# Optimization experiments

Hardware: AMD Instinct MI355X
Metric: run time of the kernel (lower is better)

Reference implementation:

```python
import jax, jax.numpy as jnp
import numpy as np

B, L, K = 256, 128, 6
FA, FB, D = 39, 10, 128
R, T = 3, 2
NEG = -9e8


def _gru(x, h, wih, whh, bih, bhh):
    # torch.nn.GRUCell semantics
    gi = x @ wih.T + bih
    gh = h @ whh.T + bhh
    ir, iz, inn = jnp.split(gi, 3, axis=-1)
    hr, hz, hn = jnp.split(gh, 3, axis=-1)
    r = jax.nn.sigmoid(ir + hr)
    z = jax.nn.sigmoid(iz + hz)
    n = jnp.tanh(inn + r * hn)
    return (1.0 - z) * n + z * h


def _forward(atom_list, bond_list, atom_mask, atom_fc_w, atom_fc_b, nbr_fc_w, nbr_fc_b,
             align_w, align_b, attend_w, attend_b, gru_wih, gru_whh, gru_bih, gru_bhh,
             mol_align_w, mol_align_b, mol_attend_w, mol_attend_b,
             mol_gru_wih, mol_gru_whh, mol_gru_bih, mol_gru_bhh, out_w, out_b,
             atom_degree_list, bond_degree_list):
    lrelu = jax.nn.leaky_relu  # slope 0.01, matches torch default
    bidx = jnp.arange(atom_list.shape[0])[:, None, None]
    gather = lambda f, idx: f[bidx, idx]  # [B,L,F] gathered by [B,L,K] -> [B,L,K,F]

    atom_feature = lrelu(atom_list @ atom_fc_w + atom_fc_b)  # [B,L,D]
    nbr = jnp.concatenate([gather(atom_list, atom_degree_list),
                           gather(bond_list, bond_degree_list)], axis=-1)
    nbr = lrelu(nbr @ nbr_fc_w + nbr_fc_b)  # [B,L,K,D]

    pad = atom_list.shape[1] - 1  # mol_length-1 is padding sentinel
    attend_mask = (atom_degree_list != pad).astype(atom_feature.dtype)[..., None]
    softmax_mask = jnp.where(atom_degree_list == pad, NEG, 0.0).astype(atom_feature.dtype)[..., None]

    def attn(cur, nbr_feat, aw, ab, tw, tb):
        exp = jnp.broadcast_to(cur[:, :, None, :], nbr_feat.shape)
        score = lrelu(jnp.concatenate([exp, nbr_feat], axis=-1) @ aw + ab) + softmax_mask
        w = jax.nn.softmax(score, axis=-2) * attend_mask  # softmax over neighbors
        return jax.nn.elu(jnp.sum(w * (nbr_feat @ tw + tb), axis=-2))

    h = atom_feature
    ctx = attn(atom_feature, nbr, align_w[0], align_b[0], attend_w[0], attend_b[0])
    h = _gru(ctx, h, gru_wih[0], gru_whh[0], gru_bih[0], gru_bhh[0])
    act = jax.nn.relu(h)
    for d in range(1, R):
        nbr_f = gather(act, atom_degree_list)
        ctx = attn(act, nbr_f, align_w[d], align_b[d], attend_w[d], attend_b[d])
        h = _gru(ctx, h, gru_wih[d], gru_whh[d], gru_bih[d], gru_bhh[d])
        act = jax.nn.relu(h)

    am = atom_mask[..., None]  # [B,L,1]
    mol_feature = jnp.sum(act * am, axis=-2)  # [B,D]
    act_mol = jax.nn.relu(mol_feature)
    mol_smask = jnp.where(am == 0, NEG, 0.0).astype(atom_feature.dtype)
    for _ in range(T):
        exp = jnp.broadcast_to(act_mol[:, None, :], act.shape)
        score = lrelu(jnp.concatenate([exp, act], axis=-1) @ mol_align_w + mol_align_b) + mol_smask
        w = jax.nn.softmax(score, axis=-2) * am  # softmax over atoms
        ctx = jax.nn.elu(jnp.sum(w * (act @ mol_attend_w + mol_attend_b), axis=-2))
        mol_feature = _gru(ctx, mol_feature, mol_gru_wih, mol_gru_whh, mol_gru_bih, mol_gru_bhh)
        act_mol = jax.nn.relu(mol_feature)
    mol_prediction = mol_feature @ out_w + out_b  # [B,1]
    return h, mol_prediction


def setup_inputs():
    key = jax.random.key(0)
    ks = jax.random.split(key, 30)
    f = lambda i, s: jax.random.normal(ks[i], s, dtype=jnp.float32) * 0.1
    return {
        'atom_list': jax.random.normal(ks[0], (B, L, FA), dtype=jnp.float32),
        'bond_list': jax.random.normal(ks[1], (B, L, FB), dtype=jnp.float32),
        'atom_mask': jnp.ones((B, L), jnp.float32),
        'atom_fc_w': f(2, (FA, D)), 'atom_fc_b': f(3, (D,)),
        'nbr_fc_w': f(4, (FA + FB, D)), 'nbr_fc_b': f(5, (D,)),
        'align_w': f(6, (R, 2 * D, 1)), 'align_b': f(7, (R, 1)),
        'attend_w': f(8, (R, D, D)), 'attend_b': f(9, (R, D)),
        'gru_wih': f(10, (R, 3 * D, D)), 'gru_whh': f(11, (R, 3 * D, D)),
        'gru_bih': f(12, (R, 3 * D)), 'gru_bhh': f(13, (R, 3 * D)),
        'mol_align_w': f(14, (2 * D, 1)), 'mol_align_b': f(15, (1,)),
        'mol_attend_w': f(16, (D, D)), 'mol_attend_b': f(17, (D,)),
        'mol_gru_wih': f(18, (3 * D, D)), 'mol_gru_whh': f(19, (3 * D, D)),
        'mol_gru_bih': f(20, (3 * D,)), 'mol_gru_bhh': f(21, (3 * D,)),
        'out_w': f(22, (D, 1)), 'out_b': f(23, (1,)),
        'atom_degree_list': jax.random.randint(ks[24], (B, L, K), 0, L),
        'bond_degree_list': jax.random.randint(ks[25], (B, L, K), 0, L),
    }


def reference(atom_list, bond_list, atom_mask, atom_fc_w, atom_fc_b, nbr_fc_w, nbr_fc_b,
              align_w, align_b, attend_w, attend_b, gru_wih, gru_whh, gru_bih, gru_bhh,
              mol_align_w, mol_align_b, mol_attend_w, mol_attend_b,
              mol_gru_wih, mol_gru_whh, mol_gru_bih, mol_gru_bhh, out_w, out_b,
              atom_degree_list, bond_degree_list):
    return _forward(atom_list, bond_list, atom_mask, atom_fc_w, atom_fc_b, nbr_fc_w, nbr_fc_b,
                    align_w, align_b, attend_w, attend_b, gru_wih, gru_whh, gru_bih, gru_bhh,
                    mol_align_w, mol_align_b, mol_attend_w, mol_attend_b,
                    mol_gru_wih, mol_gru_whh, mol_gru_bih, mol_gru_bhh, out_w, out_b,
                    atom_degree_list, bond_degree_list)
```

## Files before the change

### kernel.cpp

```cpp
#include <hip/hip_runtime.h>
#include <cstddef>


#define B_ 256
#define L_ 128
#define K_ 6
#define FA_ 39
#define FB_ 10
#define D_ 128
#define PAD_ 127
#define NEGC (-9.0e8f)
#define NA 32
#define NPAIR (NA * K_)

typedef unsigned short u16;
typedef unsigned int u32;
using s8 = __attribute__((ext_vector_type(8))) short;
using f4 = __attribute__((ext_vector_type(4))) float;

#define WIH_H 0
#define WIH_L 49152
#define WHH_H 98304
#define WHH_L 147456
#define TW_H  196608
#define TW_L  212992
#define RND_BLK2 229376
#define NB16 (3 * RND_BLK2)
#define NMOLF (2 * 128 * 384)

__device__ __forceinline__ float lrelu(float x) { return x > 0.f ? x : 0.01f * x; }
__device__ __forceinline__ float eluf(float x)  { return x > 0.f ? x : expm1f(x); }
__device__ __forceinline__ float sigm(float x)  { return 1.f / (1.f + expf(-x)); }
__device__ __forceinline__ float b2f(u16 u) {
  union { u32 i; float f; } v; v.i = ((u32)u) << 16; return v.f;
}
__device__ __forceinline__ short f2b(float f) {
  union { float f; u32 i; } v; v.f = f;
  u32 x = v.i;
  return (short)(u16)((x + 0x7FFFu + ((x >> 16) & 1u)) >> 16);
}

__global__ __launch_bounds__(256) void k_tr(
    const float* __restrict__ gwih, const float* __restrict__ gwhh,
    const float* __restrict__ attw,
    const float* __restrict__ mwih, const float* __restrict__ mwhh,
    short* __restrict__ wB, float* __restrict__ molT) {
  int idx = blockIdx.x * 256 + threadIdx.x;
  if (idx < NB16) {
    int r = idx / RND_BLK2, o = idx % RND_BLK2;
    float v; int lo;
    int e, kind;
    if (o < 98304)      { kind = 0; lo = o / 49152; e = o % 49152; }
    else if (o < 196608){ kind = 1; int o2 = o - 98304; lo = o2 / 49152; e = o2 % 49152; }
    else                { kind = 2; int o2 = o - 196608; lo = o2 / 16384; e = o2 % 16384; }
    int gt = e >> 11, rem = e & 2047;
    int kc = rem >> 9, rem2 = rem & 511;
    int lane = rem2 >> 3, j = rem2 & 7;
    int col = lane & 15, quad = lane >> 4;
    int g = gt * 16 + col;
    int k = kc * 32 + quad * 8 + j;
    if (kind == 0)      v = gwih[(size_t)r * 49152 + g * 128 + k];
    else if (kind == 1) v = gwhh[(size_t)r * 49152 + g * 128 + k];
    else                v = attw[(size_t)r * 16384 + k * 128 + g];
    short hi = f2b(v);
    wB[idx] = lo ? f2b(v - b2f((u16)hi)) : hi;
  } else if (idx < NB16 + NMOLF) {
    int e2 = idx - NB16;
    int m = e2 / 49152, e = e2 % 49152, j = e / 384, g = e % 384;
    molT[e2] = (m ? mwhh : mwih)[g * 128 + j];
  }
}

__global__ __launch_bounds__(128) void k_pre(
    const float* __restrict__ atom_list,
    const float* __restrict__ afc_w, const float* __restrict__ afc_b,
    const float* __restrict__ nbr_w,
    const float* __restrict__ aw0,
    u16* __restrict__ h0out, short* __restrict__ APg, float* __restrict__ PgA)
{
  int tid = threadIdx.x;
  int a0 = blockIdx.x * 16;
  __shared__ float xa[16 * 40];
  __shared__ float h0S[16][132];
  __shared__ float awS[128];
  __shared__ float partials[128];

  for (int i = tid; i < 16 * FA_; i += 128) {
    int a = i / FA_, c = i % FA_;
    xa[a * 40 + c] = atom_list[((size_t)(a0 + a)) * FA_ + c];
  }
  awS[tid] = aw0[tid];
  __syncthreads();

  {
    float acc[16];
    float bv = afc_b[tid];
#pragma unroll
    for (int a = 0; a < 16; a++) acc[a] = bv;
#pragma unroll 2
    for (int j = 0; j < FA_; j++) {
      float w = afc_w[j * D_ + tid];
#pragma unroll
      for (int a = 0; a < 16; a++) acc[a] += xa[a * 40 + j] * w;
    }
#pragma unroll
    for (int a = 0; a < 16; a++) {
      float hv = lrelu(acc[a]);
      h0out[(size_t)(a0 + a) * D_ + tid] = (u16)f2b(hv);
      h0S[a][tid] = hv;
    }
  }
  {
    float acc[16];
#pragma unroll
    for (int a = 0; a < 16; a++) acc[a] = 0.f;
#pragma unroll 2
    for (int j = 0; j < FA_; j++) {
      float w = nbr_w[j * D_ + tid];
#pragma unroll
      for (int a = 0; a < 16; a++) acc[a] += xa[a * 40 + j] * w;
    }
#pragma unroll
    for (int a = 0; a < 16; a++)
      APg[(size_t)(a0 + a) * D_ + tid] = f2b(acc[a]);
  }
  __syncthreads();
  {
    int a = tid >> 3, seg = tid & 7;
    float s = 0.f;
#pragma unroll
    for (int j = 0; j < 16; j++) s += h0S[a][seg * 16 + j] * awS[seg * 16 + j];
    partials[tid] = s;
  }
  __syncthreads();
  if (tid < 16) {
    float s = 0.f;
#pragma unroll
    for (int g = 0; g < 8; g++) s += partials[tid * 8 + g];
    PgA[a0 + tid] = s;
  }
}

__global__ __launch_bounds__(256) void k_q0(
    const float* __restrict__ bond_list,
    const float* __restrict__ nbr_w, const float* __restrict__ nbr_b,
    const float* __restrict__ aw0,
    const int* __restrict__ adeg, const int* __restrict__ bdeg,
    const short* __restrict__ APg, float* __restrict__ Q0g)
{
  int tid = threadIdx.x;
  __shared__ float WbS[10 * 128];
  __shared__ float nbS[128], ahS[128];
  for (int i = tid; i < 10 * 128; i += 256)
    WbS[i] = nbr_w[(FA_ + i / 128) * D_ + (i % 128)];
  if (tid < 128) { nbS[tid] = nbr_b[tid]; ahS[tid] = aw0[D_ + tid]; }
  __syncthreads();

  int p = blockIdx.x * 64 + (tid >> 2);
  int seg = tid & 3;
  int aidx = adeg[p], bidx = bdeg[p];
  int bb = p / (L_ * K_);
  const short* rowA = APg + ((size_t)bb * L_ + aidx) * D_;
  const float* brow = bond_list + ((size_t)bb * L_ + bidx) * FB_;
  float bnd[10];
#pragma unroll
  for (int m = 0; m < 10; m++) bnd[m] = brow[m];
  float s = 0.f;
  int j0 = seg * 32;
#pragma unroll 4
  for (int j = j0; j < j0 + 32; j++) {
    float v = b2f((u16)rowA[j]) + nbS[j];
#pragma unroll
    for (int m = 0; m < 10; m++) v += bnd[m] * WbS[m * 128 + j];
    s += lrelu(v) * ahS[j];
  }
  s += __shfl_xor(s, 1, 64);
  s += __shfl_xor(s, 2, 64);
  if (seg == 0) Q0g[p] = s;
}

template <int FIRST>
__global__ __launch_bounds__(512, 6) void k_round(
    const u16* __restrict__ hin,
    u16* __restrict__ hout,
    const float* __restrict__ bond_list,
    const int* __restrict__ adeg, const int* __restrict__ bdeg,
    const float* __restrict__ nbr_w, const float* __restrict__ nbr_b,
    const short* __restrict__ APg,
    const float* __restrict__ ab,
    const float* __restrict__ awN,
    const float* __restrict__ tb,
    const short* __restrict__ wR,
    const float* __restrict__ bih, const float* __restrict__ bhh,
    const float* __restrict__ Pr, const float* __restrict__ Qr,
    float* __restrict__ Pw, float* __restrict__ Qw)
{
  int tid  = threadIdx.x;
  int t128 = tid & 127;
  int hq   = tid >> 7;
  int lane = tid & 63;
  int wv   = tid >> 6;
  int quad = lane >> 4;
  int col  = lane & 15;
  int tile = (blockIdx.x & 7) * 128 + (blockIdx.x >> 3);
  int a0   = tile * NA;
  int bb   = a0 >> 7;

  const short* wihH = wR + WIH_H;
  const short* wihL = wR + WIH_L;
  const short* whhH = wR + WHH_H;
  const short* whhL = wR + WHH_L;
  const short* twH  = wR + TW_H;
  const short* twL  = wR + TW_L;

  __shared__ short hrowH[NA][136];
  __shared__ __align__(16) char arena[17408];
  __shared__ float awNS[256];
  __shared__ float partials[512];
  __shared__ float pS[NA], qS[NPAIR], wkS[NPAIR], wsS[NA];
  __shared__ int aidxS[NPAIR];
  __shared__ int bidxS[FIRST ? NPAIR : 1];
  __shared__ float bwS[FIRST ? 1920 : 1];

  short* ybarH = (short*)arena;
  short* ybarL = (short*)(arena + 8704);
  float* hnrel = (float*)arena;

  if (tid < NPAIR) {
    int av = adeg[a0 * K_ + tid];
    aidxS[tid] = av;
    if (FIRST) { bidxS[tid] = bdeg[a0 * K_ + tid]; qS[tid] = Qr[a0 * K_ + tid]; }
    else       qS[tid] = Qr[bb * L_ + av];
  } else if (tid < NPAIR + NA) {
    pS[tid - NPAIR] = Pr[a0 + (tid - NPAIR)];
  }
  if (tid < 256) awNS[tid] = awN[tid];
  __syncthreads();

  if (FIRST) {
    for (int i = tid; i < NPAIR * 10; i += 512) {
      int p = i / 10, m = i % 10;
      bwS[p * 10 + m] = bond_list[((size_t)bb * L_ + bidxS[p]) * FB_ + m];
    }
  }
#pragma unroll 4
  for (int i = 0; i < 8; i++) {
    int a = i * 4 + hq;
    hrowH[a][t128] = (short)hin[(size_t)(a0 + a) * D_ + t128];
  }
  __syncthreads();

  if (tid < NA) {
    int a = tid;
    float abv = ab[0];
    float sc[K_];
    float m = -3.0e38f;
#pragma unroll
    for (int k = 0; k < K_; k++) {
      float s = lrelu(pS[a] + qS[a * K_ + k] + abv);
      if (aidxS[a * K_ + k] == PAD_) s += NEGC;
      sc[k] = s; m = fmaxf(m, s);
    }
    float es = 0.f;
#pragma unroll
    for (int k = 0; k < K_; k++) { sc[k] = expf(sc[k] - m); es += sc[k]; }
    float ws = 0.f;
#pragma unroll
    for (int k = 0; k < K_; k++) {
      float w = (aidxS[a * K_ + k] == PAD_) ? 0.f : sc[k] / es;
      wkS[a * K_ + k] = w; ws += w;
    }
    wsS[a] = ws;
  }
  __syncthreads();

  if (FIRST) {
    const float* bondS = bwS;
    float Wreg[10];
#pragma unroll
    for (int m = 0; m < 10; m++) Wreg[m] = nbr_w[(FA_ + m) * D_ + t128];
    float nbv = nbr_b[t128];
#pragma unroll
    for (int i = 0; i < 8; i++) {
      int a = hq * 8 + i;
      float yb = 0.f;
#pragma unroll
      for (int k = 0; k < K_; k++) {
        int p = a * K_ + k;
        float nf = b2f((u16)APg[((size_t)bb * L_ + aidxS[p]) * D_ + t128]) + nbv;
#pragma unroll
        for (int m = 0; m < 10; m++) nf += bondS[p * 10 + m] * Wreg[m];
        yb += wkS[p] * lrelu(nf);
      }
      short yh = f2b(yb);
      ybarH[a * 136 + t128] = yh;
      ybarL[a * 136 + t128] = f2b(yb - b2f((u16)yh));
    }
  } else {
#pragma unroll
    for (int i = 0; i < 8; i++) {
      int a = hq * 8 + i;
      float yb = 0.f;
#pragma unroll
      for (int k = 0; k < K_; k++) {
        float v = b2f(hin[((size_t)bb * L_ + aidxS[a * K_ + k]) * D_ + t128]);
        yb += wkS[a * K_ + k] * fmaxf(v, 0.f);
      }
      short yh = f2b(yb);
      ybarH[a * 136 + t128] = yh;
      ybarL[a * 136 + t128] = f2b(yb - b2f((u16)yh));
    }
  }
  __syncthreads();

  {
    f4 c2[2] = {};
#pragma unroll
    for (int k0c = 0; k0c < 4; k0c++) {
      int fo = ((wv * 4 + k0c) * 64 + lane) * 8;
      s8 bwh = *(const s8*)&twH[fo];
      s8 bwl = *(const s8*)&twL[fo];
#pragma unroll
      for (int at = 0; at < 2; at++) {
        s8 ayh = *(const s8*)&ybarH[(at * 16 + col) * 136 + k0c * 32 + quad * 8];
        s8 ayl = *(const s8*)&ybarL[(at * 16 + col) * 136 + k0c * 32 + quad * 8];
        c2[at] = __builtin_amdgcn_mfma_f32_16x16x32_bf16(ayh, bwh, c2[at], 0, 0, 0);
        c2[at] = __builtin_amdgcn_mfma_f32_16x16x32_bf16(ayl, bwh, c2[at], 0, 0, 0);
        c2[at] = __builtin_amdgcn_mfma_f32_16x16x32_bf16(ayh, bwl, c2[at], 0, 0, 0);
      }
    }
    __syncthreads();
    int g = wv * 16 + col;
    float tbv = tb[g];
#pragma unroll
    for (int at = 0; at < 2; at++) {
#pragma unroll
      for (int r = 0; r < 4; r++) {
        int a = at * 16 + quad * 4 + r;
        float c = eluf(c2[at][r] + wsS[a] * tbv);
        short chs = f2b(c);
        ybarH[a * 136 + g] = chs;
        ybarL[a * 136 + g] = f2b(c - b2f((u16)chs));
      }
    }
  }
  __syncthreads();

  {
    const short* ctxH = ybarH;
    const short* ctxL = ybarL;
    f4 gi[2][3] = {}, gh[2][3] = {};
#pragma unroll
    for (int k0c = 0; k0c < 4; k0c++) {
      s8 ach[2], acl[2], ahh[2];
#pragma unroll
      for (int at = 0; at < 2; at++) {
        ach[at] = *(const s8*)&ctxH[(at * 16 + col) * 136 + k0c * 32 + quad * 8];
        acl[at] = *(const s8*)&ctxL[(at * 16 + col) * 136 + k0c * 32 + quad * 8];
        ahh[at] = *(const s8*)&hrowH[at * 16 + col][k0c * 32 + quad * 8];
      }
#pragma unroll
      for (int kd = 0; kd < 3; kd++) {
        int gt = wv + kd * 8;
        int fo = ((gt * 4 + k0c) * 64 + lane) * 8;
        s8 bi_h = *(const s8*)&wihH[fo];
        s8 bi_l = *(const s8*)&wihL[fo];
        s8 bh_h = *(const s8*)&whhH[fo];
        s8 bh_l = *(const s8*)&whhL[fo];
#pragma unroll
        for (int at = 0; at < 2; at++) {
          gi[at][kd] = __builtin_amdgcn_mfma_f32_16x16x32_bf16(ach[at], bi_h, gi[at][kd], 0, 0, 0);
          gi[at][kd] = __builtin_amdgcn_mfma_f32_16x16x32_bf16(acl[at], bi_h, gi[at][kd], 0, 0, 0);
          gi[at][kd] = __builtin_amdgcn_mfma_f32_16x16x32_bf16(ach[at], bi_l, gi[at][kd], 0, 0, 0);
          gh[at][kd] = __builtin_amdgcn_mfma_f32_16x16x32_bf16(ahh[at], bh_h, gh[at][kd], 0, 0, 0);
          gh[at][kd] = __builtin_amdgcn_mfma_f32_16x16x32_bf16(ahh[at], bh_l, gh[at][kd], 0, 0, 0);
        }
      }
    }
    __syncthreads();

    {
      int ic = wv * 16 + col;
      float bi0 = bih[ic], bi1 = bih[D_ + ic], bi2 = bih[2 * D_ + ic];
      float bh0 = bhh[ic], bh1 = bhh[D_ + ic], bh2 = bhh[2 * D_ + ic];
#pragma unroll
      for (int at = 0; at < 2; at++) {
#pragma unroll
        for (int r = 0; r < 4; r++) {
          int a = at * 16 + quad * 4 + r;
          float rr = sigm(gi[at][0][r] + bi0 + gh[at][0][r] + bh0);
          float zz = sigm(gi[at][1][r] + bi1 + gh[at][1][r] + bh1);
          float nn = tanhf(gi[at][2][r] + bi2 + rr * (gh[at][2][r] + bh2));
          float hv = b2f((u16)hrowH[a][ic]);
          float hn = (1.f - zz) * nn + zz * hv;
          hrowH[a][ic] = f2b(hn);
          if (Pw) hnrel[a * 132 + ic] = fmaxf(hn, 0.f);
        }
      }
    }
  }
  __syncthreads();

  {
    int a = tid >> 4, seg = tid & 15;
    *(s8*)&hout[(size_t)(a0 + a) * D_ + seg * 8] = *(const s8*)&hrowH[a][seg * 8];
  }

  if (Pw) {
    {
      int a = tid >> 4, dt = (tid >> 3) & 1, seg = tid & 7;
      float s = 0.f;
#pragma unroll
      for (int j = 0; j < 16; j++)
        s += hnrel[a * 132 + seg * 16 + j] * awNS[dt * 128 + seg * 16 + j];
      partials[tid] = s;
    }
    __syncthreads();
    if (tid < 64) {
      int a = tid >> 1, dt = tid & 1;
      float s = 0.f;
#pragma unroll
      for (int seg = 0; seg < 8; seg++) s += partials[a * 16 + dt * 8 + seg];
      if (dt) Qw[a0 + a] = s; else Pw[a0 + a] = s;
    }
  }
}

__global__ __launch_bounds__(512) void k_mol(
    const u16* __restrict__ hfin,
    float* __restrict__ hcopy,
    const float* __restrict__ amask,
    const float* __restrict__ maw, const float* __restrict__ mab,
    const float* __restrict__ mtw, const float* __restrict__ mtb,
    const float* __restrict__ wih_t, const float* __restrict__ whh_t,
    const float* __restrict__ bih, const float* __restrict__ bhh,
    const float* __restrict__ ow, const float* __restrict__ ob,
    float* __restrict__ pred)
{
  int b = blockIdx.x;
  int tid = threadIdx.x;
  int t128 = tid & 127;
  int qf = tid >> 7;
  __shared__ float actS[L_][D_ + 1];
  __shared__ float red[512];
  __shared__ float par4[4][132];
  __shared__ float pg[3][6][132];
  __shared__ float wgt[128], ybv[132], ctx[132], mfS[132], amol[132];
  __shared__ float msk[128], mawh[128], scf[128];

  if (qf == 0) { msk[t128] = amask[b * L_ + t128]; mawh[t128] = maw[D_ + t128]; }
  for (int i = 0; i < 32; i++) {
    int l = qf * 32 + i;
    float hv = b2f(hfin[(size_t)(b * L_ + l) * D_ + t128]);
    hcopy[(size_t)(b * L_ + l) * D_ + t128] = hv;
    actS[l][t128] = fmaxf(hv, 0.f);
  }
  __syncthreads();

  {
    float s = 0.f;
    for (int i = 0; i < 32; i++) { int l = qf * 32 + i; s += actS[l][t128] * msk[l]; }
    par4[qf][t128] = s;
  }
  __syncthreads();
  if (qf == 0) {
    float mf = par4[0][t128] + par4[1][t128] + par4[2][t128] + par4[3][t128];
    mfS[t128] = mf; amol[t128] = fmaxf(mf, 0.f);
  }
  __syncthreads();

  float mabv = mab[0];

  for (int t = 0; t < 2; t++) {
    red[tid] = (tid < 128) ? amol[tid] * maw[tid] : 0.f;
    __syncthreads();
    for (int s = 256; s > 0; s >>= 1) { if (tid < s) red[tid] += red[tid + s]; __syncthreads(); }
    float s0 = red[0]; __syncthreads();

    {
      float s = 0.f;
      for (int i = 0; i < 32; i++) { int j = qf * 32 + i; s += actS[t128][j] * mawh[j]; }
      par4[qf][t128] = s;
    }
    __syncthreads();
    if (qf == 0) {
      float sc = lrelu(s0 + mabv + par4[0][t128] + par4[1][t128] + par4[2][t128] + par4[3][t128]);
      if (msk[t128] == 0.f) sc += NEGC;
      scf[t128] = sc;
    }
    __syncthreads();

    float scv = scf[t128];
    red[tid] = (tid < 128) ? scv : -3.0e38f;
    __syncthreads();
    for (int s = 256; s > 0; s >>= 1) { if (tid < s) red[tid] = fmaxf(red[tid], red[tid + s]); __syncthreads(); }
    float mx = red[0]; __syncthreads();
    float e = expf(scv - mx);
    red[tid] = (tid < 128) ? e : 0.f;
    __syncthreads();
    for (int s = 256; s > 0; s >>= 1) { if (tid < s) red[tid] += red[tid + s]; __syncthreads(); }
    float es = red[0]; __syncthreads();
    float w = (e / es) * msk[t128];
    if (qf == 0) wgt[t128] = w;
    red[tid] = (tid < 128) ? w : 0.f;
    __syncthreads();
    for (int s = 256; s > 0; s >>= 1) { if (tid < s) red[tid] += red[tid + s]; __syncthreads(); }
    float wsum = red[0]; __syncthreads();

    {
      float s = 0.f;
      for (int i = 0; i < 32; i++) { int l = qf * 32 + i; s += wgt[l] * actS[l][t128]; }
      par4[qf][t128] = s;
    }
    __syncthreads();
    if (qf == 0) ybv[t128] = par4[0][t128] + par4[1][t128] + par4[2][t128] + par4[3][t128];
    __syncthreads();

    {
      float s = 0.f;
#pragma unroll 2
      for (int i = 0; i < 32; i++) { int j = qf * 32 + i; s += ybv[j] * mtw[j * D_ + t128]; }
      par4[qf][t128] = s;
    }
    __syncthreads();
    if (qf == 0)
      ctx[t128] = eluf(par4[0][t128] + par4[1][t128] + par4[2][t128] + par4[3][t128]
                       + wsum * mtb[t128]);
    __syncthreads();

    {
      float gi0 = 0, gi1 = 0, gi2 = 0, gh0 = 0, gh1 = 0, gh2 = 0;
#pragma unroll 2
      for (int i = 0; i < 32; i++) {
        int j = qf * 32 + i;
        const float* wi = wih_t + (size_t)j * 384;
        const float* wh = whh_t + (size_t)j * 384;
        float xc = ctx[j], xh = mfS[j];
        gi0 += xc * wi[t128]; gi1 += xc * wi[128 + t128]; gi2 += xc * wi[256 + t128];
        gh0 += xh * wh[t128]; gh1 += xh * wh[128 + t128]; gh2 += xh * wh[256 + t128];
      }
      if (qf > 0) {
        pg[qf - 1][0][t128] = gi0; pg[qf - 1][1][t128] = gi1; pg[qf - 1][2][t128] = gi2;
        pg[qf - 1][3][t128] = gh0; pg[qf - 1][4][t128] = gh1; pg[qf - 1][5][t128] = gh2;
      }
      __syncthreads();
      if (qf == 0) {
        gi0 += pg[0][0][t128] + pg[1][0][t128] + pg[2][0][t128] + bih[t128];
        gi1 += pg[0][1][t128] + pg[1][1][t128] + pg[2][1][t128] + bih[128 + t128];
        gi2 += pg[0][2][t128] + pg[1][2][t128] + pg[2][2][t128] + bih[256 + t128];
        gh0 += pg[0][3][t128] + pg[1][3][t128] + pg[2][3][t128] + bhh[t128];
        gh1 += pg[0][4][t128] + pg[1][4][t128] + pg[2][4][t128] + bhh[128 + t128];
        gh2 += pg[0][5][t128] + pg[1][5][t128] + pg[2][5][t128] + bhh[256 + t128];
        float r = sigm(gi0 + gh0);
        float z = sigm(gi1 + gh1);
        float n = tanhf(gi2 + r * gh2);
        float hn = (1.f - z) * n + z * mfS[t128];
        mfS[t128] = hn;
        amol[t128] = fmaxf(hn, 0.f);
      }
      __syncthreads();
    }
  }

  red[tid] = (tid < 128) ? mfS[tid] * ow[tid] : 0.f;
  __syncthreads();
  for (int s = 256; s > 0; s >>= 1) { if (tid < s) red[tid] += red[tid + s]; __syncthreads(); }
  if (tid == 0) pred[b] = red[0] + ob[0];
}

extern "C" void kernel_launch(void* const* d_in, const int* in_sizes, int n_in,
                              void* d_out, int out_size, void* d_ws, size_t ws_size,
                              hipStream_t stream) {
  const float* atom_list    = (const float*)d_in[0];
  const float* bond_list    = (const float*)d_in[1];
  const float* atom_mask    = (const float*)d_in[2];
  const float* atom_fc_w    = (const float*)d_in[3];
  const float* atom_fc_b    = (const float*)d_in[4];
  const float* nbr_fc_w     = (const float*)d_in[5];
  const float* nbr_fc_b     = (const float*)d_in[6];
  const float* align_w      = (const float*)d_in[7];
  const float* align_b      = (const float*)d_in[8];
  const float* attend_w     = (const float*)d_in[9];
  const float* attend_b     = (const float*)d_in[10];
  const float* gru_wih      = (const float*)d_in[11];
  const float* gru_whh      = (const float*)d_in[12];
  const float* gru_bih      = (const float*)d_in[13];
  const float* gru_bhh      = (const float*)d_in[14];
  const float* mol_align_w  = (const float*)d_in[15];
  const float* mol_align_b  = (const float*)d_in[16];
  const float* mol_attend_w = (const float*)d_in[17];
  const float* mol_attend_b = (const float*)d_in[18];
  const float* mol_gru_wih  = (const float*)d_in[19];
  const float* mol_gru_whh  = (const float*)d_in[20];
  const float* mol_gru_bih  = (const float*)d_in[21];
  const float* mol_gru_bhh  = (const float*)d_in[22];
  const float* out_w        = (const float*)d_in[23];
  const float* out_b        = (const float*)d_in[24];
  const int*   adeg         = (const int*)d_in[25];
  const int*   bdeg         = (const int*)d_in[26];

  const size_t NH = (size_t)B_ * L_ * D_;
  u16*   hA   = (u16*)d_ws;
  u16*   hB   = hA + NH;
  short* wB   = (short*)(hB + NH);
  float* molT = (float*)(wB + NB16);
  float* PgA  = molT + NMOLF;
  float* QgA  = PgA + B_ * L_;
  float* PgB  = QgA + B_ * L_;
  float* QgB  = PgB + B_ * L_;
  short* APg  = (short*)(QgB + B_ * L_);
  float* Q0g  = (float*)(APg + NH);
  float* hOut = (float*)d_out;
  float* pred = hOut + NH;

  k_tr<<<dim3((NB16 + NMOLF + 255) / 256), dim3(256), 0, stream>>>(
      gru_wih, gru_whh, attend_w, mol_gru_wih, mol_gru_whh, wB, molT);

  k_pre<<<dim3(B_ * L_ / 16), dim3(128), 0, stream>>>(
      atom_list, atom_fc_w, atom_fc_b, nbr_fc_w, align_w, hA, APg, PgA);
  k_q0<<<dim3(B_ * L_ * K_ / 64), dim3(256), 0, stream>>>(
      bond_list, nbr_fc_w, nbr_fc_b, align_w, adeg, bdeg, APg, Q0g);

  dim3 blk(512), grd(B_ * L_ / NA);

  k_round<1><<<grd, blk, 0, stream>>>(
      hA, hB, bond_list, adeg, bdeg, nbr_fc_w, nbr_fc_b, APg,
      align_b, align_w + 2 * D_, attend_b,
      wB + 0 * (size_t)RND_BLK2, gru_bih, gru_bhh,
      PgA, Q0g, PgB, QgB);
  k_round<0><<<grd, blk, 0, stream>>>(
      hB, hA, bond_list, adeg, bdeg, nbr_fc_w, nbr_fc_b, APg,
      align_b + 1, align_w + 4 * D_, attend_b + D_,
      wB + 1 * (size_t)RND_BLK2, gru_bih + 3 * D_, gru_bhh + 3 * D_,
      PgB, QgB, PgA, QgA);
  k_round<0><<<grd, blk, 0, stream>>>(
      hA, hB, bond_list, adeg, bdeg, nbr_fc_w, nbr_fc_b, APg,
      align_b + 2, align_w + 4 * D_, attend_b + 2 * D_,
      wB + 2 * (size_t)RND_BLK2, gru_bih + 6 * D_, gru_bhh + 6 * D_,
      PgA, QgA, (float*)nullptr, (float*)nullptr);

  k_mol<<<dim3(B_), dim3(512), 0, stream>>>(
      hB, hOut, atom_mask, mol_align_w, mol_align_b, mol_attend_w, mol_attend_b,
      molT, molT + 128 * 384,
      mol_gru_bih, mol_gru_bhh, out_w, out_b, pred);
}
```

Before: 361.8 us.

## Vectorize neighbor gathers per thread and use wavefront shuffle reductions

Threads now own 8 contiguous feature channels of one atom, so neighbor and h-row gathers use 16-byte vector loads, and the ybar hi/lo writes to shared memory are vectorized. One __syncthreads after the h-row copy is dropped because a later barrier covers it. The mol kernel's log-step shared-memory tree reductions become wave shuffle reductions with a two-element shared buffer, and the launch-bounds occupancy hint drops from 6 to 4 blocks, giving more registers per thread. The aim is fewer memory instructions and fewer barriers, at the cost of higher register pressure from the per-thread 10x4 weight arrays.

```diff
diff --git a/kernel.cpp b/kernel.cpp
--- a/kernel.cpp
+++ b/kernel.cpp
@@ -180,7 +180,7 @@
 }
 
 template <int FIRST>
-__global__ __launch_bounds__(512, 6) void k_round(
+__global__ __launch_bounds__(512, 4) void k_round(
     const u16* __restrict__ hin,
     u16* __restrict__ hout,
     const float* __restrict__ bond_list,
@@ -196,12 +196,12 @@
     float* __restrict__ Pw, float* __restrict__ Qw)
 {
   int tid  = threadIdx.x;
-  int t128 = tid & 127;
-  int hq   = tid >> 7;
   int lane = tid & 63;
   int wv   = tid >> 6;
   int quad = lane >> 4;
   int col  = lane & 15;
+  int aT   = tid >> 4;
+  int dg   = (tid & 15) * 8;
   int tile = (blockIdx.x & 7) * 128 + (blockIdx.x >> 3);
   int a0   = tile * NA;
   int bb   = a0 >> 7;
@@ -243,12 +243,7 @@
       bwS[p * 10 + m] = bond_list[((size_t)bb * L_ + bidxS[p]) * FB_ + m];
     }
   }
-#pragma unroll 4
-  for (int i = 0; i < 8; i++) {
-    int a = i * 4 + hq;
-    hrowH[a][t128] = (short)hin[(size_t)(a0 + a) * D_ + t128];
-  }
-  __syncthreads();
+  *(s8*)&hrowH[aT][dg] = *(const s8*)&hin[(size_t)(a0 + aT) * D_ + dg];
 
   if (tid < NA) {
     int a = tid;
@@ -274,42 +269,57 @@
   }
   __syncthreads();
 
-  if (FIRST) {
-    const float* bondS = bwS;
-    float Wreg[10];
-#pragma unroll
-    for (int m = 0; m < 10; m++) Wreg[m] = nbr_w[(FA_ + m) * D_ + t128];
-    float nbv = nbr_b[t128];
-#pragma unroll
-    for (int i = 0; i < 8; i++) {
-      int a = hq * 8 + i;
-      float yb = 0.f;
+  {
+    float yb[8];
+#pragma unroll
+    for (int j = 0; j < 8; j++) yb[j] = 0.f;
+    if (FIRST) {
+#pragma unroll
+      for (int h = 0; h < 2; h++) {
+        float Wr[10][4];
+#pragma unroll
+        for (int m = 0; m < 10; m++) {
+          float4 w = *(const float4*)&nbr_w[(FA_ + m) * D_ + dg + h * 4];
+          Wr[m][0] = w.x; Wr[m][1] = w.y; Wr[m][2] = w.z; Wr[m][3] = w.w;
+        }
+        float4 nb4 = *(const float4*)&nbr_b[dg + h * 4];
+        float nb[4] = {nb4.x, nb4.y, nb4.z, nb4.w};
+#pragma unroll
+        for (int k = 0; k < K_; k++) {
+          int p = aT * K_ + k;
+          ushort4 ap4 = *(const ushort4*)&APg[((size_t)bb * L_ + aidxS[p]) * D_ + dg + h * 4];
+          float nf[4] = { b2f(ap4.x) + nb[0], b2f(ap4.y) + nb[1],
+                          b2f(ap4.z) + nb[2], b2f(ap4.w) + nb[3] };
+#pragma unroll
+          for (int m = 0; m < 10; m++) {
+            float bv = bwS[p * 10 + m];
+#pragma unroll
+            for (int j = 0; j < 4; j++) nf[j] += bv * Wr[m][j];
+          }
+          float w = wkS[p];
+#pragma unroll
+          for (int j = 0; j < 4; j++) yb[h * 4 + j] += w * lrelu(nf[j]);
+        }
+      }
+    } else {
 #pragma unroll
       for (int k = 0; k < K_; k++) {
-        int p = a * K_ + k;
-        float nf = b2f((u16)APg[((size_t)bb * L_ + aidxS[p]) * D_ + t128]) + nbv;
-#pragma unroll
-        for (int m = 0; m < 10; m++) nf += bondS[p * 10 + m] * Wreg[m];
-        yb += wkS[p] * lrelu(nf);
-      }
-      short yh = f2b(yb);
-      ybarH[a * 136 + t128] = yh;
-      ybarL[a * 136 + t128] = f2b(yb - b2f((u16)yh));
-    }
-  } else {
-#pragma unroll
-    for (int i = 0; i < 8; i++) {
-      int a = hq * 8 + i;
-      float yb = 0.f;
-#pragma unroll
-      for (int k = 0; k < K_; k++) {
-        float v = b2f(hin[((size_t)bb * L_ + aidxS[a * K_ + k]) * D_ + t128]);
-        yb += wkS[a * K_ + k] * fmaxf(v, 0.f);
-      }
-      short yh = f2b(yb);
-      ybarH[a * 136 + t128] = yh;
-      ybarL[a * 136 + t128] = f2b(yb - b2f((u16)yh));
-    }
+        int p = aT * K_ + k;
+        float w = wkS[p];
+        s8 hv8 = *(const s8*)&hin[((size_t)bb * L_ + aidxS[p]) * D_ + dg];
+#pragma unroll
+        for (int j = 0; j < 8; j++) yb[j] += w * fmaxf(b2f((u16)hv8[j]), 0.f);
+      }
+    }
+    s8 yh8, yl8;
+#pragma unroll
+    for (int j = 0; j < 8; j++) {
+      short hi = f2b(yb[j]);
+      yh8[j] = hi;
+      yl8[j] = f2b(yb[j] - b2f((u16)hi));
+    }
+    *(s8*)&ybarH[aT * 136 + dg] = yh8;
+    *(s8*)&ybarL[aT * 136 + dg] = yl8;
   }
   __syncthreads();
 
@@ -401,10 +411,7 @@
   }
   __syncthreads();
 
-  {
-    int a = tid >> 4, seg = tid & 15;
-    *(s8*)&hout[(size_t)(a0 + a) * D_ + seg * 8] = *(const s8*)&hrowH[a][seg * 8];
-  }
+  *(s8*)&hout[(size_t)(a0 + aT) * D_ + dg] = *(const s8*)&hrowH[aT][dg];
 
   if (Pw) {
     {
@@ -424,6 +431,29 @@
       if (dt) Qw[a0 + a] = s; else Pw[a0 + a] = s;
     }
   }
+}
+
+__device__ __forceinline__ float blk_sum128(float v, int tid, float* redS) {
+  if (tid < 128) {
+#pragma unroll
+    for (int s = 1; s < 64; s <<= 1) v += __shfl_xor(v, s, 64);
+    if ((tid & 63) == 0) redS[tid >> 6] = v;
+  }
+  __syncthreads();
+  float r = redS[0] + redS[1];
+  __syncthreads();
+  return r;
+}
+__device__ __forceinline__ float blk_max128(float v, int tid, float* redS) {
+  if (tid < 128) {
+#pragma unroll
+    for (int s = 1; s < 64; s <<= 1) v = fmaxf(v, __shfl_xor(v, s, 64));
+    if ((tid & 63) == 0) redS[tid >> 6] = v;
+  }
+  __syncthreads();
+  float r = fmaxf(redS[0], redS[1]);
+  __syncthreads();
+  return r;
 }
 
 __global__ __launch_bounds__(512) void k_mol(
@@ -442,7 +472,7 @@
   int t128 = tid & 127;
   int qf = tid >> 7;
   __shared__ float actS[L_][D_ + 1];
-  __shared__ float red[512];
+  __shared__ float redS[2];
   __shared__ float par4[4][132];
   __shared__ float pg[3][6][132];
   __shared__ float wgt[128], ybv[132], ctx[132], mfS[132], amol[132];
@@ -472,10 +502,7 @@
   float mabv = mab[0];
 
   for (int t = 0; t < 2; t++) {
-    red[tid] = (tid < 128) ? amol[tid] * maw[tid] : 0.f;
-    __syncthreads();
-    for (int s = 256; s > 0; s >>= 1) { if (tid < s) red[tid] += red[tid + s]; __syncthreads(); }
-    float s0 = red[0]; __syncthreads();
+    float s0 = blk_sum128((tid < 128) ? amol[tid] * maw[tid] : 0.f, tid, redS);
 
     {
       float s = 0.f;
@@ -491,21 +518,12 @@
     __syncthreads();
 
     float scv = scf[t128];
-    red[tid] = (tid < 128) ? scv : -3.0e38f;
-    __syncthreads();
-    for (int s = 256; s > 0; s >>= 1) { if (tid < s) red[tid] = fmaxf(red[tid], red[tid + s]); __syncthreads(); }
-    float mx = red[0]; __syncthreads();
+    float mx = blk_max128((tid < 128) ? scv : -3.0e38f, tid, redS);
     float e = expf(scv - mx);
-    red[tid] = (tid < 128) ? e : 0.f;
-    __syncthreads();
-    for (int s = 256; s > 0; s >>= 1) { if (tid < s) red[tid] += red[tid + s]; __syncthreads(); }
-    float es = red[0]; __syncthreads();
+    float es = blk_sum128((tid < 128) ? e : 0.f, tid, redS);
     float w = (e / es) * msk[t128];
     if (qf == 0) wgt[t128] = w;
-    red[tid] = (tid < 128) ? w : 0.f;
-    __syncthreads();
-    for (int s = 256; s > 0; s >>= 1) { if (tid < s) red[tid] += red[tid + s]; __syncthreads(); }
-    float wsum = red[0]; __syncthreads();
+    float wsum = blk_sum128((tid < 128) ? w : 0.f, tid, redS);
 
     {
       float s = 0.f;
@@ -562,10 +580,8 @@
     }
   }
 
-  red[tid] = (tid < 128) ? mfS[tid] * ow[tid] : 0.f;
-  __syncthreads();
-  for (int s = 256; s > 0; s >>= 1) { if (tid < s) red[tid] += red[tid + s]; __syncthreads(); }
-  if (tid == 0) pred[b] = red[0] + ob[0];
+  float fin = blk_sum128((tid < 128) ? mfS[tid] * ow[tid] : 0.f, tid, redS);
+  if (tid == 0) pred[b] = fin + ob[0];
 }
 
 extern "C" void kernel_launch(void* const* d_in, const int* in_sizes, int n_in,
```

Result: faster. 328.2 us (-9.3%).
